# Optimization experiments

Measured on AMD Instinct MI355X. Metric: run time of the kernel, lower is better.

## Reference

```python
import jax, jax.numpy as jnp
import numpy as np

S = 3        # num_scale
C = 256      # codebook / feature dim
K = 512      # codebook size


def _bilinear_down(x, f):
    # torch F.interpolate(scale_factor=1/f, mode='bilinear', align_corners=False)
    # for even integer f: src = (i+0.5)*f - 0.5 = f*i + (f//2 - 1) + 0.5 -> avg of 2 neighbors.
    o = f // 2 - 1
    x = (x[:, :, o::f, :] + x[:, :, o + 1::f, :]) * 0.5
    x = (x[:, :, :, o::f] + x[:, :, :, o + 1::f]) * 0.5
    return x


def _encode(img, w, b):
    # stride-4 patchify conv: (b,3,H,W) -> (b,C,H/4,W/4), NCHW
    y = jax.lax.conv_general_dilated(img, w, (4, 4), 'VALID',
                                     dimension_numbers=('NCHW', 'OIHW', 'NCHW'))
    return y + b[None, :, None, None]


def _match(e, cb):
    # e [..., c], cb [K, c]. logits = -||e - cb||^2; zsoft = softmax(logits).
    # Only max-prob and argmax are consumed downstream, so compute them stably.
    d = (jnp.sum(e * e, -1, keepdims=True)
         - 2.0 * jnp.einsum('...c,kc->...k', e, cb)
         + jnp.sum(cb * cb, -1))
    logits = -d
    zidx = jnp.argmax(logits, -1)
    maxprob = jnp.exp(jnp.max(logits, -1) - jax.scipy.special.logsumexp(logits, -1))
    return maxprob, zidx


def _resample(e, j, i):
    # e is NHWC at scale j; bring it to scale i (avg_pool if j<i, nearest upsample if j>i)
    if j == i:
        return e
    if j < i:
        f = 2 ** (i - j)
        b, h, w, c = e.shape
        return e.reshape(b, h // f, f, w // f, f, c).mean(axis=(2, 4))
    f = 2 ** (j - i)
    return jnp.repeat(jnp.repeat(e, f, axis=1), f, axis=2)


def setup_inputs() -> dict:
    key = jax.random.key(0)
    k1, k2, k3 = jax.random.split(key, 3)
    image = jax.random.normal(k1, (8, 3, 256, 256), jnp.float32)
    conv_w = jax.random.normal(k2, (C, 3, 4, 4), jnp.float32) * 0.05
    conv_b = jnp.zeros((C,), jnp.float32)
    codebooks = jax.random.normal(k3, (1 + S, K, C), jnp.float32) * 0.05
    return {"image": image, "conv_w": conv_w, "conv_b": conv_b, "codebooks": codebooks}


def reference(image, conv_w, conv_b, codebooks):
    # multi-scale inputs (bilinear downsample), shared encoder per scale
    imgs = [image] + [_bilinear_down(image, 2 ** k) for k in range(1, S)]
    encodes = [_encode(im, conv_w, conv_b) for im in imgs]          # NCHW, sizes 64/32/16
    enc_nhwc = [jnp.transpose(e, (0, 2, 3, 1)) for e in encodes]

    cb0 = codebooks[0]
    # ms_fuse, scale i1 = 0 (only scale 0 is returned when decode=None, retr=True):
    stack = jnp.stack([_resample(enc_nhwc[j], j, 0) for j in range(S)])  # [s,b,h,w,c]
    prob1, idx1 = _match(stack, cb0)                                      # [s,b,h,w]
    sel = jnp.argmax(prob1, 0)                                            # [b,h,w] best scale
    zidx1 = jnp.take_along_axis(idx1, sel[None], 0)[0]                    # [b,h,w]
    enc1 = jnp.take_along_axis(stack, sel[None, ..., None], 0)[0]         # [b,h,w,c]
    quant1 = cb0[zidx1]

    # per-scale quantizer for scale 0
    _, zidx2 = _match(enc_nhwc[0], codebooks[1])
    quant2 = codebooks[1][zidx2]

    zidx0 = jnp.stack([zidx1, zidx2], -1)            # [b,h,w,2]
    e_fused = (enc1 + enc_nhwc[0]) * 0.5
    q_fused = (quant1 + quant2) * 0.5
    # alpha = 0 -> residual == quant; naive STE
    ste0 = e_fused + jax.lax.stop_gradient(q_fused - e_fused)

    return (encodes[0],
            jnp.transpose(zidx0, (0, 3, 1, 2)),
            jnp.transpose(ste0, (0, 3, 1, 2)))
```

## Files before the change

### kernel.cpp

```cpp
#include <hip/hip_runtime.h>
#include <math.h>


#define FEAT_OFF   0
#define PART_OFF   11010048
#define PROB_OFF   13434880
#define IDX1_OFF   13477888
#define IDX2_OFF   13520896
#define CNF_OFF    13553664
#define CND_OFF    13554688
#define CBS_OFF    13556736
#define IMG1_OFF   13818880
#define IMG2_OFF   14212096
#define RLIST_OFF  14310400
#define DLIST_OFF  14386176
#define CNT_OFF    14418944

#define PLANE_STRIDE 11010048

#define EPS_V 1e-3f
#define EPS_P_REL 2e-3f

typedef __attribute__((ext_vector_type(8))) short short8;
typedef __attribute__((ext_vector_type(4))) float f32x4;

__device__ inline unsigned short f2bf(float x) {
    unsigned u = __float_as_uint(x);
    return (unsigned short)((u + 0x7FFFu + ((u >> 16) & 1u)) >> 16);
}
__device__ inline float bf2f(unsigned short h) {
    return __uint_as_float(((unsigned)h) << 16);
}
__device__ inline int rswz(int row) { return (row & 3) ^ ((row >> 2) & 3); }

__device__ inline void glds16(const unsigned short* g, unsigned short* l) {
    __builtin_amdgcn_global_load_lds(
        (const __attribute__((address_space(1))) void*)g,
        (__attribute__((address_space(3))) void*)l, 16, 0, 0);
}

__launch_bounds__(256)
__global__ void prep(const float* __restrict__ image,
                     const float* __restrict__ codebooks,
                     float* __restrict__ img1, float* __restrict__ img2,
                     double* __restrict__ cnd, float* __restrict__ cnf,
                     unsigned short* __restrict__ cbs, int* __restrict__ cnt) {
    int bid = blockIdx.x, tid = threadIdx.x;
    if (bid == 0 && tid < 2) cnt[tid] = 0;
    if (bid < 1536) {
        int i = bid * 256 + tid;
        int x = i & 127;
        int t = i >> 7;
        int y = t & 127;
        int bc = t >> 7;
        const float* base = image + ((size_t)bc * 256 + (size_t)(y * 2)) * 256;
        int cx = x * 2;
        float v00 = base[cx],     v10 = base[256 + cx];
        float v01 = base[cx + 1], v11 = base[256 + cx + 1];
        img1[i] = ((v00 + v10) * 0.5f + (v01 + v11) * 0.5f) * 0.5f;
    } else if (bid < 1920) {
        int i = (bid - 1536) * 256 + tid;
        int x = i & 63;
        int t = i >> 6;
        int y = t & 63;
        int bc = t >> 6;
        const float* base = image + ((size_t)bc * 256 + (size_t)(y * 4 + 1)) * 256;
        int cx = x * 4 + 1;
        float v00 = base[cx],     v10 = base[256 + cx];
        float v01 = base[cx + 1], v11 = base[256 + cx + 1];
        img2[i] = ((v00 + v10) * 0.5f + (v01 + v11) * 0.5f) * 0.5f;
    } else if (bid < 2176) {
        int row = (bid - 1920) * 4 + (tid >> 6);
        int lane = tid & 63;
        const float* p = codebooks + (size_t)row * 256;
        double s = 0.0;
        for (int c = lane; c < 256; c += 64) {
            double v = (double)p[c];
            s = fma(v, v, s);
        }
        #pragma unroll
        for (int off = 32; off; off >>= 1) s += __shfl_down(s, off);
        if (lane == 0) { cnd[row] = s; cnf[row] = (float)s; }
    } else {
        int i = (bid - 2176) * 256 + tid;
        int book = i >> 17, rem = i & 131071;
        int code = rem >> 8, ch = rem & 255;
        float c = codebooks[(size_t)book * 131072 + rem];
        unsigned short h0 = f2bf(c);
        unsigned short h1 = f2bf(c - bf2f(h0));
        int codeblk = code >> 7, row = code & 127;
        int kc = ch >> 5, q = (ch >> 3) & 3, j = ch & 7;
        int qs = q ^ rswz(row);
        size_t off = ((((size_t)(book * 2) * 4 + codeblk) * 8 + kc) * 128 + row) * 32 + qs * 8 + j;
        cbs[off] = h0;
        cbs[off + 4 * 32768] = h1;
    }
}

__launch_bounds__(256)
__global__ void encode_all(const float* __restrict__ image,
                           const float* __restrict__ img1,
                           const float* __restrict__ img2,
                           const float* __restrict__ w,
                           const float* __restrict__ bias,
                           float* __restrict__ feat,
                           unsigned short* __restrict__ featbf) {
    __shared__ float patch[12 * 128];
    __shared__ __align__(16) unsigned short pk[2][4][2][256];
    int bid = blockIdx.x;
    const float* img; int Hout, rowbase, local, xbase, npos, Wimg, WL, colbase;
    if (bid < 1024) {
        img = image; Hout = 64; rowbase = 0;
        local = bid >> 1; int half = bid & 1;
        xbase = half * 32; npos = 32; Wimg = 256; WL = 128; colbase = half * 128;
    } else if (bid < 1280) {
        img = img1; Hout = 32; rowbase = 32768;
        local = bid - 1024; xbase = 0; npos = 32; Wimg = 128; WL = 128; colbase = 0;
    } else {
        img = img2; Hout = 16; rowbase = 40960;
        local = bid - 1280; xbase = 0; npos = 16; Wimg = 64; WL = 64; colbase = 0;
    }
    int Wout = Hout;
    int tid = threadIdx.x;
    int b = local / Hout, y = local % Hout;
    int Himg = Hout * 4;

    const float* ibase = img + (size_t)b * 3 * Himg * Wimg;
    int nload = 12 * WL;
    for (int i = tid; i < nload; i += 256) {
        int cl = i % WL, r = i / WL;
        int ci = r >> 2, kh = r & 3;
        patch[r * WL + cl] = ibase[((size_t)ci * Himg + 4 * y + kh) * Wimg + colbase + cl];
    }
    float wr[48];
    #pragma unroll
    for (int j = 0; j < 48; j++) wr[j] = w[tid * 48 + j];
    float bv = bias[tid];
    __syncthreads();

    int fp = tid >> 6, fwp = (tid >> 5) & 1, fkc = (tid >> 2) & 7, fwg = tid & 3;
    int rb = rowbase + (b * Hout + y) * Wout + xbase;
    for (int x0 = 0; x0 < npos; x0 += 4) {
        int buf = (x0 >> 2) & 1;
        #pragma unroll
        for (int p = 0; p < 4; p++) {
            int xl = x0 + p;
            float acc = 0.f;
            #pragma unroll
            for (int ci = 0; ci < 3; ci++)
                #pragma unroll
                for (int kh = 0; kh < 4; kh++) {
                    const float* pr = &patch[(ci * 4 + kh) * WL + 4 * xl];
                    #pragma unroll
                    for (int kw = 0; kw < 4; kw++)
                        acc = fmaf(pr[kw], wr[ci * 16 + kh * 4 + kw], acc);
                }
            float val = acc + bv;
            feat[(size_t)(rb + xl) * 256 + tid] = val;
            unsigned short hi = f2bf(val);
            pk[buf][p][0][tid] = hi;
            pk[buf][p][1][tid] = f2bf(val - bf2f(hi));
        }
        __syncthreads();
        {
            int r = rb + x0 + fp;
            int rowblk = r >> 7, rrow = r & 127;
            int ch0 = fkc * 32 + ((fwg ^ rswz(rrow)) << 3);
            uint4 v = *(const uint4*)&pk[buf][fp][fwp][ch0];
            size_t off = (((size_t)rowblk * 8 + fkc) * 128 + rrow) * 32 + fwg * 8
                       + (size_t)fwp * PLANE_STRIDE;
            *(uint4*)&featbf[off] = v;
        }
    }
}

__launch_bounds__(256, 2)
__global__ void match_bulk(const unsigned short* __restrict__ featbf,
                           const unsigned short* __restrict__ cbs,
                           const float* __restrict__ cnf,
                           float* __restrict__ partials) {
    __shared__ unsigned short A0s[2][4096], A1s[2][4096], B0s[2][4096], B1s[2][4096];
    int bid0 = blockIdx.x;
    int bid = (bid0 & 7) * 296 + (bid0 >> 3);
    int codeblk = bid & 3, rowtile = bid >> 2;
    int book = (rowtile >= 336) ? 1 : 0;
    int rowblk = book ? rowtile - 336 : rowtile;
    int vr0 = rowtile * 128;
    int tid = threadIdx.x;
    int wid = tid >> 6, l = tid & 63;
    int waveY = wid & 1, waveX = wid >> 1;
    int lm = l & 15, lq = l >> 4;
    int slot = lq ^ rswz(lm);
    int wlds = wid * 512;

    f32x4 acc[4][4];
    #pragma unroll
    for (int ct = 0; ct < 4; ct++)
        #pragma unroll
        for (int rt = 0; rt < 4; rt++) acc[ct][rt] = (f32x4)0.0f;

    const unsigned short* gA0 = featbf + (size_t)rowblk * 32768 + tid * 8;
    const unsigned short* gA1 = gA0 + PLANE_STRIDE;
    const unsigned short* gB0 = cbs + ((size_t)(book * 8) + codeblk) * 32768 + tid * 8;
    const unsigned short* gB1 = gB0 + 4 * 32768;

    auto STAGE = [&](int buf, int kc) {
        const unsigned short* ga0 = gA0 + kc * 4096;
        const unsigned short* ga1 = gA1 + kc * 4096;
        const unsigned short* gb0 = gB0 + kc * 4096;
        const unsigned short* gb1 = gB1 + kc * 4096;
        #pragma unroll
        for (int i = 0; i < 2; i++) {
            glds16(ga0 + i * 2048, &A0s[buf][i * 2048 + wlds]);
            glds16(ga1 + i * 2048, &A1s[buf][i * 2048 + wlds]);
            glds16(gb0 + i * 2048, &B0s[buf][i * 2048 + wlds]);
            glds16(gb1 + i * 2048, &B1s[buf][i * 2048 + wlds]);
        }
    };

    short8 a0[4], a1[4], b0[4], b1[4];
    auto LOADFRAG = [&](int cur) {
        #pragma unroll
        for (int t = 0; t < 4; t++) {
            int ra = (waveY * 64 + t * 16 + lm) * 32 + slot * 8;
            int rbx = (waveX * 64 + t * 16 + lm) * 32 + slot * 8;
            a0[t] = *(const short8*)&A0s[cur][ra];
            a1[t] = *(const short8*)&A1s[cur][ra];
            b0[t] = *(const short8*)&B0s[cur][rbx];
            b1[t] = *(const short8*)&B1s[cur][rbx];
        }
    };
    auto DOMFMA = [&]() {
        __builtin_amdgcn_s_setprio(1);
        #pragma unroll
        for (int ct = 0; ct < 4; ct++)
            #pragma unroll
            for (int rt = 0; rt < 4; rt++) {
                acc[ct][rt] = __builtin_amdgcn_mfma_f32_16x16x32_bf16(b0[ct], a0[rt], acc[ct][rt], 0, 0, 0);
                acc[ct][rt] = __builtin_amdgcn_mfma_f32_16x16x32_bf16(b1[ct], a0[rt], acc[ct][rt], 0, 0, 0);
                acc[ct][rt] = __builtin_amdgcn_mfma_f32_16x16x32_bf16(b0[ct], a1[rt], acc[ct][rt], 0, 0, 0);
            }
        __builtin_amdgcn_s_setprio(0);
    };

    STAGE(0, 0);
    STAGE(1, 1);

#define MB_STEP(KC)                                                        \
    do {                                                                   \
        asm volatile("s_waitcnt vmcnt(8)" ::: "memory");                   \
        __builtin_amdgcn_s_barrier();                                      \
        __builtin_amdgcn_sched_barrier(0);                                 \
        LOADFRAG((KC) & 1);                                                \
        asm volatile("s_waitcnt lgkmcnt(0)" ::: "memory");                 \
        __builtin_amdgcn_sched_barrier(0);                                 \
        __builtin_amdgcn_s_barrier();                                      \
        __builtin_amdgcn_sched_barrier(0);                                 \
        STAGE((KC) & 1, (KC) + 2);                                         \
        DOMFMA();                                                          \
    } while (0)

    MB_STEP(0); MB_STEP(1); MB_STEP(2); MB_STEP(3); MB_STEP(4); MB_STEP(5);
#undef MB_STEP

    asm volatile("s_waitcnt vmcnt(8)" ::: "memory");
    __builtin_amdgcn_s_barrier();
    __builtin_amdgcn_sched_barrier(0);
    LOADFRAG(0);
    asm volatile("s_waitcnt lgkmcnt(0)" ::: "memory");
    __builtin_amdgcn_sched_barrier(0);
    DOMFMA();
    asm volatile("s_waitcnt vmcnt(0)" ::: "memory");
    __builtin_amdgcn_s_barrier();
    __builtin_amdgcn_sched_barrier(0);
    LOADFRAG(1);
    asm volatile("s_waitcnt lgkmcnt(0)" ::: "memory");
    __builtin_amdgcn_sched_barrier(0);
    DOMFMA();

    int kbase = codeblk * 128 + waveX * 64 + lq * 4;
    float4 cnv4[4];
    #pragma unroll
    for (int ct = 0; ct < 4; ct++)
        cnv4[ct] = *(const float4*)&cnf[book * 512 + kbase + ct * 16];
    float4* part4 = (float4*)partials;

    #pragma unroll
    for (int rt = 0; rt < 4; rt++) {
        float v[4][4];
        #pragma unroll
        for (int ct = 0; ct < 4; ct++) {
            v[ct][0] = 2.0f * acc[ct][rt][0] - cnv4[ct].x;
            v[ct][1] = 2.0f * acc[ct][rt][1] - cnv4[ct].y;
            v[ct][2] = 2.0f * acc[ct][rt][2] - cnv4[ct].z;
            v[ct][3] = 2.0f * acc[ct][rt][3] - cnv4[ct].w;
        }
        float m1 = v[0][0], m2 = -3.4e38f;
        int k1 = kbase;
        #pragma unroll
        for (int ct = 0; ct < 4; ct++)
            #pragma unroll
            for (int j = 0; j < 4; j++) {
                if (ct == 0 && j == 0) continue;
                float val = v[ct][j];
                if (val > m1) { m2 = m1; m1 = val; k1 = kbase + ct * 16 + j; }
                else m2 = fmaxf(m2, val);
            }
        #pragma unroll
        for (int off = 16; off < 64; off <<= 1) {
            float mo1 = __shfl_xor(m1, off);
            float mo2 = __shfl_xor(m2, off);
            int ko1 = __shfl_xor(k1, off);
            if (mo1 > m1 || (mo1 == m1 && ko1 < k1)) { m2 = fmaxf(m1, mo2); m1 = mo1; k1 = ko1; }
            else m2 = fmaxf(m2, mo1);
        }
        float s = 0.f;
        if (!book) {
            #pragma unroll
            for (int ct = 0; ct < 4; ct++)
                #pragma unroll
                for (int j = 0; j < 4; j++) s += __expf(v[ct][j] - m1);
            #pragma unroll
            for (int off = 16; off < 64; off <<= 1) s += __shfl_xor(s, off);
        }
        if (lq == 0) {
            int vr = vr0 + waveY * 64 + rt * 16 + lm;
            float4 st = make_float4(m1, m2, __int_as_float(k1), s);
            part4[(size_t)vr * 8 + codeblk * 2 + waveX] = st;
        }
    }
}

__global__ void combine_rows(const float* __restrict__ partials,
                             int* __restrict__ idx1, int* __restrict__ idx2,
                             float* __restrict__ prob,
                             int* __restrict__ rlist, int* __restrict__ cnt) {
    int vr = blockIdx.x * 256 + threadIdx.x;
    const float4* p = (const float4*)partials + (size_t)vr * 8;
    float sm[8], ss[8];
    float4 a = p[0];
    float m1 = a.x, m2 = a.y; int k1 = __float_as_int(a.z);
    sm[0] = a.x; ss[0] = a.w;
    #pragma unroll
    for (int j = 1; j < 8; j++) {
        float4 b = p[j];
        sm[j] = b.x; ss[j] = b.w;
        int kk = __float_as_int(b.z);
        if (b.x > m1 || (b.x == m1 && kk < k1)) { m2 = fmaxf(m1, b.y); m1 = b.x; k1 = kk; }
        else m2 = fmaxf(m2, b.x);
    }
    float S = 0.f;
    #pragma unroll
    for (int j = 0; j < 8; j++) S += ss[j] * __expf(sm[j] - m1);
    if (vr < 43008) { idx1[vr] = k1; prob[vr] = 1.0f / S; }
    else idx2[vr - 43008] = k1;
    if (m1 - m2 < EPS_V) { int pos = atomicAdd(cnt, 1); rlist[pos] = vr; }
}

__launch_bounds__(256)
__global__ void rescue_exact(const float* __restrict__ feat,
                             const float* __restrict__ codebooks,
                             const double* __restrict__ cnd,
                             const int* __restrict__ rlist, const int* __restrict__ cnt,
                             int* __restrict__ idx1, int* __restrict__ idx2,
                             float* __restrict__ prob) {
    __shared__ double sfd[256];
    __shared__ double rv[4]; __shared__ int rk[4]; __shared__ double rs[4];
    __shared__ double gvmax; __shared__ int gkmax;
    int tid = threadIdx.x;
    int lane = tid & 63, wave = tid >> 6;
    int n = cnt[0];
    for (int e = blockIdx.x; e < n; e += gridDim.x) {
        int vr = rlist[e];
        int book = vr >= 43008;
        int fr = book ? vr - 43008 : vr;
        sfd[tid] = (double)feat[(size_t)fr * 256 + tid];
        __syncthreads();
        const float* cb = codebooks + (size_t)book * 131072;
        double vloc[2]; int kk[2];
        #pragma unroll
        for (int h = 0; h < 2; h++) {
            int k = h * 256 + tid;
            const float* cp = cb + (size_t)k * 256;
            double d0 = 0.0, d1 = 0.0, d2 = 0.0, d3 = 0.0;
            for (int c = 0; c < 256; c += 4) {
                float4 cv = *(const float4*)&cp[c];
                d0 = fma((double)cv.x, sfd[c],     d0);
                d1 = fma((double)cv.y, sfd[c + 1], d1);
                d2 = fma((double)cv.z, sfd[c + 2], d2);
                d3 = fma((double)cv.w, sfd[c + 3], d3);
            }
            double dot = (d0 + d1) + (d2 + d3);
            vloc[h] = 2.0 * dot - cnd[book * 512 + k];
            kk[h] = k;
        }
        double bv = vloc[0]; int bk = kk[0];
        if (vloc[1] > bv || (vloc[1] == bv && kk[1] < bk)) { bv = vloc[1]; bk = kk[1]; }
        #pragma unroll
        for (int off = 32; off; off >>= 1) {
            double vo = __shfl_xor(bv, off);
            int ko = __shfl_xor(bk, off);
            if (vo > bv || (vo == bv && ko < bk)) { bv = vo; bk = ko; }
        }
        if (lane == 0) { rv[wave] = bv; rk[wave] = bk; }
        __syncthreads();
        if (tid == 0) {
            double v0 = rv[0]; int K = rk[0];
            #pragma unroll
            for (int w = 1; w < 4; w++)
                if (rv[w] > v0 || (rv[w] == v0 && rk[w] < K)) { v0 = rv[w]; K = rk[w]; }
            gvmax = v0; gkmax = K;
        }
        __syncthreads();
        double vm = gvmax;
        double s = exp(vloc[0] - vm) + exp(vloc[1] - vm);
        #pragma unroll
        for (int off = 32; off; off >>= 1) s += __shfl_xor(s, off);
        if (lane == 0) rs[wave] = s;
        __syncthreads();
        if (tid == 0) {
            double S = ((rs[0] + rs[1]) + rs[2]) + rs[3];
            if (book) idx2[fr] = gkmax;
            else { idx1[vr] = gkmax; prob[vr] = (float)(1.0 / S); }
        }
        __syncthreads();
    }
}

__launch_bounds__(256)
__global__ void fuse1(const float* __restrict__ feat,
                      const float* __restrict__ prob,
                      const int* __restrict__ idx1, const int* __restrict__ idx2,
                      const float* __restrict__ codebooks,
                      float* __restrict__ out0, float* __restrict__ outZ,
                      float* __restrict__ outS,
                      int* __restrict__ dlist, int* __restrict__ cnt) {
    __shared__ int rsel_s[64], i1_s[64], i2_s[64], defer_s[64];
    int tid = threadIdx.x;
    int bid = blockIdx.x;
    int chh = bid & 1;
    int rowid = bid >> 1;
    int b = rowid >> 6, y = rowid & 63;

    if (tid < 64) {
        int x = tid;
        int r0 = (b * 64 + y) * 64 + x;
        int r1 = 32768 + (b * 32 + (y >> 1)) * 32 + (x >> 1);
        int r2 = 40960 + (b * 16 + (y >> 2)) * 16 + (x >> 2);
        float p0 = prob[r0], p1 = prob[r1], p2 = prob[r2];
        int rsel = r0; float best = p0;
        if (p1 > best) { best = p1; rsel = r1; }
        if (p2 > best) { best = p2; rsel = r2; }
        float second = (rsel == r0) ? fmaxf(p1, p2)
                     : (rsel == r1) ? fmaxf(p0, p2) : fmaxf(p0, p1);
        int defer = (best - second < EPS_P_REL * best) ? 1 : 0;
        defer_s[x] = defer;
        if (defer) {
            if (chh == 0) {
                int pos = atomicAdd(cnt + 1, 1);
                dlist[pos] = (b << 12) | (y << 6) | x;
            }
            rsel_s[x] = r0; i1_s[x] = 0; i2_s[x] = 0;
        } else {
            int i1 = idx1[rsel], i2 = idx2[r0];
            rsel_s[x] = rsel; i1_s[x] = i1; i2_s[x] = i2;
            if (chh == 0) {
                size_t zb = (size_t)b * 8192 + (size_t)y * 64 + x;
                outZ[zb] = (float)i1;
                outZ[zb + 4096] = (float)i2;
            }
        }
    }
    __syncthreads();

    int x = tid & 63, cc = tid >> 6;
    int r0 = (b * 64 + y) * 64 + x;
    const float* e0p = feat + (size_t)r0 * 256;
    const float* e1p = feat + (size_t)rsel_s[x] * 256;
    const float* q1p = codebooks + (size_t)i1_s[x] * 256;
    const float* q2p = codebooks + (size_t)(512 + i2_s[x]) * 256;
    int defer = defer_s[x];
    for (int it = 0; it < 8; it++) {
        int c = chh * 128 + it * 16 + cc * 4;
        float4 e0 = *(const float4*)&e0p[c];
        size_t o = (((size_t)b * 256 + c) * 64 + y) * 64 + x;
        out0[o]         = e0.x;
        out0[o + 4096]  = e0.y;
        out0[o + 8192]  = e0.z;
        out0[o + 12288] = e0.w;
        if (!defer) {
            float4 e1 = *(const float4*)&e1p[c];
            float4 q1 = *(const float4*)&q1p[c];
            float4 q2 = *(const float4*)&q2p[c];
            float ef, qf;
            ef = (e1.x + e0.x) * 0.5f; qf = (q1.x + q2.x) * 0.5f; outS[o]         = ef + (qf - ef);
            ef = (e1.y + e0.y) * 0.5f; qf = (q1.y + q2.y) * 0.5f; outS[o + 4096]  = ef + (qf - ef);
            ef = (e1.z + e0.z) * 0.5f; qf = (q1.z + q2.z) * 0.5f; outS[o + 8192]  = ef + (qf - ef);
            ef = (e1.w + e0.w) * 0.5f; qf = (q1.w + q2.w) * 0.5f; outS[o + 12288] = ef + (qf - ef);
        }
    }
}

__launch_bounds__(256)
__global__ void fuse2(const float* __restrict__ feat,
                      const float* __restrict__ codebooks,
                      const double* __restrict__ cnd,
                      const int* __restrict__ idx2,
                      const int* __restrict__ dlist, const int* __restrict__ cnt,
                      float* __restrict__ outZ, float* __restrict__ outS) {
    __shared__ double sfd[256];
    __shared__ double rv[4]; __shared__ int rk[4]; __shared__ double rs[4];
    __shared__ double gvmax;
    __shared__ double pRes[3]; __shared__ int kRes[3];
    __shared__ int selS, i2S;
    int tid = threadIdx.x;
    int lane = tid & 63, wave = tid >> 6;
    int n = cnt[1];
    for (int e = blockIdx.x; e < n; e += gridDim.x) {
        int px = dlist[e];
        int b = px >> 12, y = (px >> 6) & 63, x = px & 63;
        int r0 = (b * 64 + y) * 64 + x;
        int r1 = 32768 + (b * 32 + (y >> 1)) * 32 + (x >> 1);
        int r2 = 40960 + (b * 16 + (y >> 2)) * 16 + (x >> 2);
        int rows[3] = {r0, r1, r2};
        for (int s3 = 0; s3 < 3; s3++) {
            sfd[tid] = (double)feat[(size_t)rows[s3] * 256 + tid];
            __syncthreads();
            double vloc[2];
            #pragma unroll
            for (int h = 0; h < 2; h++) {
                int k = h * 256 + tid;
                const float* cp = codebooks + (size_t)k * 256;
                double d0 = 0.0, d1 = 0.0, d2 = 0.0, d3 = 0.0;
                for (int c = 0; c < 256; c += 4) {
                    float4 cv = *(const float4*)&cp[c];
                    d0 = fma((double)cv.x, sfd[c],     d0);
                    d1 = fma((double)cv.y, sfd[c + 1], d1);
                    d2 = fma((double)cv.z, sfd[c + 2], d2);
                    d3 = fma((double)cv.w, sfd[c + 3], d3);
                }
                double dot = (d0 + d1) + (d2 + d3);
                vloc[h] = 2.0 * dot - cnd[k];
            }
            double bv = vloc[0]; int bk = tid;
            if (vloc[1] > bv) { bv = vloc[1]; bk = tid + 256; }
            #pragma unroll
            for (int off = 32; off; off >>= 1) {
                double vo = __shfl_xor(bv, off);
                int ko = __shfl_xor(bk, off);
                if (vo > bv || (vo == bv && ko < bk)) { bv = vo; bk = ko; }
            }
            if (lane == 0) { rv[wave] = bv; rk[wave] = bk; }
            __syncthreads();
            if (tid == 0) {
                double v0 = rv[0]; int K = rk[0];
                #pragma unroll
                for (int w = 1; w < 4; w++)
                    if (rv[w] > v0 || (rv[w] == v0 && rk[w] < K)) { v0 = rv[w]; K = rk[w]; }
                gvmax = v0; kRes[s3] = K;
            }
            __syncthreads();
            double vm = gvmax;
            double s = exp(vloc[0] - vm) + exp(vloc[1] - vm);
            #pragma unroll
            for (int off = 32; off; off >>= 1) s += __shfl_xor(s, off);
            if (lane == 0) rs[wave] = s;
            __syncthreads();
            if (tid == 0) pRes[s3] = 1.0 / (((rs[0] + rs[1]) + rs[2]) + rs[3]);
            __syncthreads();
        }
        if (tid == 0) {
            int sel = 0; double best = pRes[0];
            if (pRes[1] > best) { best = pRes[1]; sel = 1; }
            if (pRes[2] > best) { best = pRes[2]; sel = 2; }
            selS = sel;
            int i2 = idx2[r0];
            i2S = i2;
            size_t zb = (size_t)b * 8192 + (size_t)y * 64 + x;
            outZ[zb] = (float)kRes[sel];
            outZ[zb + 4096] = (float)i2;
        }
        __syncthreads();
        int sel = selS;
        int c = tid;
        float e0 = feat[(size_t)r0 * 256 + c];
        float e1 = feat[(size_t)rows[sel] * 256 + c];
        float q1 = codebooks[(size_t)kRes[sel] * 256 + c];
        float q2 = codebooks[(size_t)(512 + i2S) * 256 + c];
        float ef = (e1 + e0) * 0.5f;
        float qf = (q1 + q2) * 0.5f;
        size_t o = (((size_t)b * 256 + c) * 64 + y) * 64 + x;
        outS[o] = ef + (qf - ef);
        __syncthreads();
    }
}

extern "C" void kernel_launch(void* const* d_in, const int* in_sizes, int n_in,
                              void* d_out, int out_size, void* d_ws, size_t ws_size,
                              hipStream_t stream) {
    (void)in_sizes; (void)n_in; (void)out_size; (void)ws_size;
    const float* image     = (const float*)d_in[0];
    const float* conv_w    = (const float*)d_in[1];
    const float* conv_b    = (const float*)d_in[2];
    const float* codebooks = (const float*)d_in[3];

    float*  ws    = (float*)d_ws;
    float*  feat  = ws + FEAT_OFF;
    float*  parts = ws + PART_OFF;
    float*  prob  = ws + PROB_OFF;
    int*    idx1  = (int*)(ws + IDX1_OFF);
    int*    idx2  = (int*)(ws + IDX2_OFF);
    float*  cnf   = ws + CNF_OFF;
    double* cnd   = (double*)(ws + CND_OFF);
    unsigned short* cbs = (unsigned short*)(ws + CBS_OFF);
    float*  img1  = ws + IMG1_OFF;
    float*  img2  = ws + IMG2_OFF;
    int*    rlist = (int*)(ws + RLIST_OFF);
    int*    dlist = (int*)(ws + DLIST_OFF);
    int*    cnt   = (int*)(ws + CNT_OFF);

    float* out  = (float*)d_out;
    float* out0 = out;
    float* outZ = out + 8388608;
    float* outS = out + 8454144;
    unsigned short* featbf = (unsigned short*)d_out;

    prep<<<3200, 256, 0, stream>>>(image, codebooks, img1, img2, cnd, cnf, cbs, cnt);
    encode_all<<<1408, 256, 0, stream>>>(image, img1, img2, conv_w, conv_b, feat, featbf);
    match_bulk<<<2368, 256, 0, stream>>>(featbf, cbs, cnf, parts);
    combine_rows<<<296, 256, 0, stream>>>(parts, idx1, idx2, prob, rlist, cnt);
    rescue_exact<<<1024, 256, 0, stream>>>(feat, codebooks, cnd, rlist, cnt, idx1, idx2, prob);
    fuse1<<<1024, 256, 0, stream>>>(feat, prob, idx1, idx2, codebooks, out0, outZ, outS, dlist, cnt);
    fuse2<<<512, 256, 0, stream>>>(feat, codebooks, cnd, idx2, dlist, cnt, outZ, outS);
}
```

Baseline: 291.7 us.

## Write scale-0 features straight to NCHW output and drop the fp32 feature buffer

```diff
diff --git a/kernel.cpp b/kernel.cpp
--- a/kernel.cpp
+++ b/kernel.cpp
@@ -2,7 +2,8 @@
 #include <math.h>
 
 
-#define FEAT_OFF   0
+#define FEAT12_OFF 0
+#define FBLO_OFF   2621440
 #define PART_OFF   11010048
 #define PROB_OFF   13434880
 #define IDX1_OFF   13477888
@@ -16,8 +17,6 @@
 #define DLIST_OFF  14386176
 #define CNT_OFF    14418944
 
-#define PLANE_STRIDE 11010048
-
 #define EPS_V 1e-3f
 #define EPS_P_REL 2e-3f
 
@@ -37,6 +36,16 @@
     __builtin_amdgcn_global_load_lds(
         (const __attribute__((address_space(1))) void*)g,
         (__attribute__((address_space(3))) void*)l, 16, 0, 0);
+}
+
+__device__ inline float feat_elem(const float* __restrict__ out0,
+                                  const float* __restrict__ feat12,
+                                  int fr, int c) {
+    if (fr < 32768) {
+        int b = fr >> 12, y = (fr >> 6) & 63, x = fr & 63;
+        return out0[(((size_t)b * 256 + c) * 64 + y) * 64 + x];
+    }
+    return feat12[(size_t)(fr - 32768) * 256 + c];
 }
 
 __launch_bounds__(256)
@@ -103,14 +112,18 @@
                            const float* __restrict__ img2,
                            const float* __restrict__ w,
                            const float* __restrict__ bias,
-                           float* __restrict__ feat,
-                           unsigned short* __restrict__ featbf) {
+                           float* __restrict__ feat12,
+                           unsigned short* __restrict__ fbh,
+                           unsigned short* __restrict__ fbl,
+                           float* __restrict__ out0) {
     __shared__ float patch[12 * 128];
-    __shared__ __align__(16) unsigned short pk[2][4][2][256];
+    __shared__ __align__(16) unsigned short pk[2][8][2][256];
+    __shared__ __align__(16) float vf[2][8][256];
     int bid = blockIdx.x;
     const float* img; int Hout, rowbase, local, xbase, npos, Wimg, WL, colbase;
+    int isS0 = 0;
     if (bid < 1024) {
-        img = image; Hout = 64; rowbase = 0;
+        img = image; Hout = 64; rowbase = 0; isS0 = 1;
         local = bid >> 1; int half = bid & 1;
         xbase = half * 32; npos = 32; Wimg = 256; WL = 128; colbase = half * 128;
     } else if (bid < 1280) {
@@ -138,12 +151,11 @@
     float bv = bias[tid];
     __syncthreads();
 
-    int fp = tid >> 6, fwp = (tid >> 5) & 1, fkc = (tid >> 2) & 7, fwg = tid & 3;
     int rb = rowbase + (b * Hout + y) * Wout + xbase;
-    for (int x0 = 0; x0 < npos; x0 += 4) {
-        int buf = (x0 >> 2) & 1;
-        #pragma unroll
-        for (int p = 0; p < 4; p++) {
+    for (int x0 = 0; x0 < npos; x0 += 8) {
+        int buf = (x0 >> 3) & 1;
+        #pragma unroll
+        for (int p = 0; p < 8; p++) {
             int xl = x0 + p;
             float acc = 0.f;
             #pragma unroll
@@ -156,26 +168,39 @@
                         acc = fmaf(pr[kw], wr[ci * 16 + kh * 4 + kw], acc);
                 }
             float val = acc + bv;
-            feat[(size_t)(rb + xl) * 256 + tid] = val;
             unsigned short hi = f2bf(val);
             pk[buf][p][0][tid] = hi;
             pk[buf][p][1][tid] = f2bf(val - bf2f(hi));
-        }
-        __syncthreads();
-        {
+            vf[buf][p][tid] = val;
+            if (!isS0) feat12[(size_t)(rb + xl - 32768) * 256 + tid] = val;
+        }
+        __syncthreads();
+        #pragma unroll
+        for (int s = tid; s < 512; s += 256) {
+            int fp = s >> 6; int rest = s & 63;
+            int fwp = rest >> 5, fkc = (rest >> 2) & 7, fwg = rest & 3;
             int r = rb + x0 + fp;
             int rowblk = r >> 7, rrow = r & 127;
             int ch0 = fkc * 32 + ((fwg ^ rswz(rrow)) << 3);
             uint4 v = *(const uint4*)&pk[buf][fp][fwp][ch0];
-            size_t off = (((size_t)rowblk * 8 + fkc) * 128 + rrow) * 32 + fwg * 8
-                       + (size_t)fwp * PLANE_STRIDE;
-            *(uint4*)&featbf[off] = v;
+            size_t off = (((size_t)rowblk * 8 + fkc) * 128 + rrow) * 32 + fwg * 8;
+            if (fwp) *(uint4*)&fbl[off] = v;
+            else     *(uint4*)&fbh[off] = v;
+        }
+        if (isS0) {
+            int c = tid;
+            size_t o = (((size_t)b * 256 + c) * 64 + y) * 64 + (xbase + x0);
+            float4 v0 = make_float4(vf[buf][0][c], vf[buf][1][c], vf[buf][2][c], vf[buf][3][c]);
+            float4 v1 = make_float4(vf[buf][4][c], vf[buf][5][c], vf[buf][6][c], vf[buf][7][c]);
+            *(float4*)&out0[o]     = v0;
+            *(float4*)&out0[o + 4] = v1;
         }
     }
 }
 
 __launch_bounds__(256, 2)
-__global__ void match_bulk(const unsigned short* __restrict__ featbf,
+__global__ void match_bulk(const unsigned short* __restrict__ fbh,
+                           const unsigned short* __restrict__ fbl,
                            const unsigned short* __restrict__ cbs,
                            const float* __restrict__ cnf,
                            float* __restrict__ partials) {
@@ -199,8 +224,8 @@
         #pragma unroll
         for (int rt = 0; rt < 4; rt++) acc[ct][rt] = (f32x4)0.0f;
 
-    const unsigned short* gA0 = featbf + (size_t)rowblk * 32768 + tid * 8;
-    const unsigned short* gA1 = gA0 + PLANE_STRIDE;
+    const unsigned short* gA0 = fbh + (size_t)rowblk * 32768 + tid * 8;
+    const unsigned short* gA1 = fbl + (size_t)rowblk * 32768 + tid * 8;
     const unsigned short* gB0 = cbs + ((size_t)(book * 8) + codeblk) * 32768 + tid * 8;
     const unsigned short* gB1 = gB0 + 4 * 32768;
 
@@ -358,7 +383,8 @@
 }
 
 __launch_bounds__(256)
-__global__ void rescue_exact(const float* __restrict__ feat,
+__global__ void rescue_exact(const float* __restrict__ out0,
+                             const float* __restrict__ feat12,
                              const float* __restrict__ codebooks,
                              const double* __restrict__ cnd,
                              const int* __restrict__ rlist, const int* __restrict__ cnt,
@@ -374,7 +400,7 @@
         int vr = rlist[e];
         int book = vr >= 43008;
         int fr = book ? vr - 43008 : vr;
-        sfd[tid] = (double)feat[(size_t)fr * 256 + tid];
+        sfd[tid] = (double)feat_elem(out0, feat12, fr, tid);
         __syncthreads();
         const float* cb = codebooks + (size_t)book * 131072;
         double vloc[2]; int kk[2];
@@ -428,14 +454,12 @@
 }
 
 __launch_bounds__(256)
-__global__ void fuse1(const float* __restrict__ feat,
-                      const float* __restrict__ prob,
+__global__ void fuse1(const float* __restrict__ prob,
                       const int* __restrict__ idx1, const int* __restrict__ idx2,
                       const float* __restrict__ codebooks,
-                      float* __restrict__ out0, float* __restrict__ outZ,
-                      float* __restrict__ outS,
+                      float* __restrict__ outZ, float* __restrict__ outS,
                       int* __restrict__ dlist, int* __restrict__ cnt) {
-    __shared__ int rsel_s[64], i1_s[64], i2_s[64], defer_s[64];
+    __shared__ int i1_s[64], i2_s[64], defer_s[64];
     int tid = threadIdx.x;
     int bid = blockIdx.x;
     int chh = bid & 1;
@@ -460,10 +484,10 @@
                 int pos = atomicAdd(cnt + 1, 1);
                 dlist[pos] = (b << 12) | (y << 6) | x;
             }
-            rsel_s[x] = r0; i1_s[x] = 0; i2_s[x] = 0;
+            i1_s[x] = 0; i2_s[x] = 0;
         } else {
             int i1 = idx1[rsel], i2 = idx2[r0];
-            rsel_s[x] = rsel; i1_s[x] = i1; i2_s[x] = i2;
+            i1_s[x] = i1; i2_s[x] = i2;
             if (chh == 0) {
                 size_t zb = (size_t)b * 8192 + (size_t)y * 64 + x;
                 outZ[zb] = (float)i1;
@@ -474,35 +498,25 @@
     __syncthreads();
 
     int x = tid & 63, cc = tid >> 6;
-    int r0 = (b * 64 + y) * 64 + x;
-    const float* e0p = feat + (size_t)r0 * 256;
-    const float* e1p = feat + (size_t)rsel_s[x] * 256;
     const float* q1p = codebooks + (size_t)i1_s[x] * 256;
     const float* q2p = codebooks + (size_t)(512 + i2_s[x]) * 256;
-    int defer = defer_s[x];
+    if (defer_s[x]) return;
+    #pragma unroll
     for (int it = 0; it < 8; it++) {
         int c = chh * 128 + it * 16 + cc * 4;
-        float4 e0 = *(const float4*)&e0p[c];
+        float4 q1 = *(const float4*)&q1p[c];
+        float4 q2 = *(const float4*)&q2p[c];
         size_t o = (((size_t)b * 256 + c) * 64 + y) * 64 + x;
-        out0[o]         = e0.x;
-        out0[o + 4096]  = e0.y;
-        out0[o + 8192]  = e0.z;
-        out0[o + 12288] = e0.w;
-        if (!defer) {
-            float4 e1 = *(const float4*)&e1p[c];
-            float4 q1 = *(const float4*)&q1p[c];
-            float4 q2 = *(const float4*)&q2p[c];
-            float ef, qf;
-            ef = (e1.x + e0.x) * 0.5f; qf = (q1.x + q2.x) * 0.5f; outS[o]         = ef + (qf - ef);
-            ef = (e1.y + e0.y) * 0.5f; qf = (q1.y + q2.y) * 0.5f; outS[o + 4096]  = ef + (qf - ef);
-            ef = (e1.z + e0.z) * 0.5f; qf = (q1.z + q2.z) * 0.5f; outS[o + 8192]  = ef + (qf - ef);
-            ef = (e1.w + e0.w) * 0.5f; qf = (q1.w + q2.w) * 0.5f; outS[o + 12288] = ef + (qf - ef);
-        }
+        outS[o]         = (q1.x + q2.x) * 0.5f;
+        outS[o + 4096]  = (q1.y + q2.y) * 0.5f;
+        outS[o + 8192]  = (q1.z + q2.z) * 0.5f;
+        outS[o + 12288] = (q1.w + q2.w) * 0.5f;
     }
 }
 
 __launch_bounds__(256)
-__global__ void fuse2(const float* __restrict__ feat,
+__global__ void fuse2(const float* __restrict__ out0,
+                      const float* __restrict__ feat12,
                       const float* __restrict__ codebooks,
                       const double* __restrict__ cnd,
                       const int* __restrict__ idx2,
@@ -524,7 +538,7 @@
         int r2 = 40960 + (b * 16 + (y >> 2)) * 16 + (x >> 2);
         int rows[3] = {r0, r1, r2};
         for (int s3 = 0; s3 < 3; s3++) {
-            sfd[tid] = (double)feat[(size_t)rows[s3] * 256 + tid];
+            sfd[tid] = (double)feat_elem(out0, feat12, rows[s3], tid);
             __syncthreads();
             double vloc[2];
             #pragma unroll
@@ -583,14 +597,10 @@
         __syncthreads();
         int sel = selS;
         int c = tid;
-        float e0 = feat[(size_t)r0 * 256 + c];
-        float e1 = feat[(size_t)rows[sel] * 256 + c];
         float q1 = codebooks[(size_t)kRes[sel] * 256 + c];
         float q2 = codebooks[(size_t)(512 + i2S) * 256 + c];
-        float ef = (e1 + e0) * 0.5f;
-        float qf = (q1 + q2) * 0.5f;
         size_t o = (((size_t)b * 256 + c) * 64 + y) * 64 + x;
-        outS[o] = ef + (qf - ef);
+        outS[o] = (q1 + q2) * 0.5f;
         __syncthreads();
     }
 }
@@ -604,32 +614,36 @@
     const float* conv_b    = (const float*)d_in[2];
     const float* codebooks = (const float*)d_in[3];
 
-    float*  ws    = (float*)d_ws;
-    float*  feat  = ws + FEAT_OFF;
-    float*  parts = ws + PART_OFF;
-    float*  prob  = ws + PROB_OFF;
-    int*    idx1  = (int*)(ws + IDX1_OFF);
-    int*    idx2  = (int*)(ws + IDX2_OFF);
-    float*  cnf   = ws + CNF_OFF;
-    double* cnd   = (double*)(ws + CND_OFF);
+    float*  ws     = (float*)d_ws;
+    float*  feat12 = ws + FEAT12_OFF;
+    unsigned short* fbl = (unsigned short*)(ws + FBLO_OFF);
+    float*  parts  = ws + PART_OFF;
+    float*  prob   = ws + PROB_OFF;
+    int*    idx1   = (int*)(ws + IDX1_OFF);
+    int*    idx2   = (int*)(ws + IDX2_OFF);
+    float*  cnf    = ws + CNF_OFF;
+    double* cnd    = (double*)(ws + CND_OFF);
     unsigned short* cbs = (unsigned short*)(ws + CBS_OFF);
-    float*  img1  = ws + IMG1_OFF;
-    float*  img2  = ws + IMG2_OFF;
-    int*    rlist = (int*)(ws + RLIST_OFF);
-    int*    dlist = (int*)(ws + DLIST_OFF);
-    int*    cnt   = (int*)(ws + CNT_OFF);
+    float*  img1   = ws + IMG1_OFF;
+    float*  img2   = ws + IMG2_OFF;
+    int*    rlist  = (int*)(ws + RLIST_OFF);
+    int*    dlist  = (int*)(ws + DLIST_OFF);
+    int*    cnt    = (int*)(ws + CNT_OFF);
 
     float* out  = (float*)d_out;
     float* out0 = out;
     float* outZ = out + 8388608;
     float* outS = out + 8454144;
-    unsigned short* featbf = (unsigned short*)d_out;
+    unsigned short* fbh = (unsigned short*)outS;
 
     prep<<<3200, 256, 0, stream>>>(image, codebooks, img1, img2, cnd, cnf, cbs, cnt);
-    encode_all<<<1408, 256, 0, stream>>>(image, img1, img2, conv_w, conv_b, feat, featbf);
-    match_bulk<<<2368, 256, 0, stream>>>(featbf, cbs, cnf, parts);
+    encode_all<<<1408, 256, 0, stream>>>(image, img1, img2, conv_w, conv_b,
+                                         feat12, fbh, fbl, out0);
+    match_bulk<<<2368, 256, 0, stream>>>(fbh, fbl, cbs, cnf, parts);
     combine_rows<<<296, 256, 0, stream>>>(parts, idx1, idx2, prob, rlist, cnt);
-    rescue_exact<<<1024, 256, 0, stream>>>(feat, codebooks, cnd, rlist, cnt, idx1, idx2, prob);
-    fuse1<<<1024, 256, 0, stream>>>(feat, prob, idx1, idx2, codebooks, out0, outZ, outS, dlist, cnt);
-    fuse2<<<512, 256, 0, stream>>>(feat, codebooks, cnd, idx2, dlist, cnt, outZ, outS);
-}
+    rescue_exact<<<1024, 256, 0, stream>>>(out0, feat12, codebooks, cnd, rlist, cnt,
+                                           idx1, idx2, prob);
+    fuse1<<<1024, 256, 0, stream>>>(prob, idx1, idx2, codebooks, outZ, outS, dlist, cnt);
+    fuse2<<<512, 256, 0, stream>>>(out0, feat12, codebooks, cnd, idx2, dlist, cnt,
+                                   outZ, outS);
+}
```

New measurement: 277.9 us. 4.7% less time.
